# Optimization experiments

Hardware: AMD Instinct MI355X
Metric: run time of the kernel (lower is better)

Reference implementation:

```python
import jax, jax.numpy as jnp
import numpy as np

N = 50000      # nodes
E = 800000     # edges (avg degree 16)
H = 4          # attention heads
F_IN = 256     # input feature dim
D = 64         # per-head hidden/out dim (hidden*H = 256 chains into next layer)
NEG_SLOPE = 0.2  # DGL GATConv default leaky_relu slope


def setup_inputs() -> dict:
    key = jax.random.key(0)
    ks = jax.random.split(key, 12)
    inp = {
        "features": jax.random.normal(ks[0], (N, F_IN), jnp.float32),
        "src": jax.random.randint(ks[1], (E,), 0, N, jnp.int32),
        "dst": jax.random.randint(ks[2], (E,), 0, N, jnp.int32),
    }
    dims = [(F_IN, D), (H * D, D), (H * D, D)]
    for i, (fin, dout) in enumerate(dims):
        sc = 1.0 / np.sqrt(fin)
        inp[f"W{i+1}"] = jax.random.normal(ks[3 + 3 * i], (fin, H * dout), jnp.float32) * sc
        inp[f"al{i+1}"] = jax.random.normal(ks[4 + 3 * i], (H, dout), jnp.float32) * 0.1
        inp[f"ar{i+1}"] = jax.random.normal(ks[5 + 3 * i], (H, dout), jnp.float32) * 0.1
        inp[f"b{i+1}"] = jnp.zeros((H * dout,), jnp.float32)
    return inp


def gat_layer(h, src, dst, W, al, ar, b, act):
    n = h.shape[0]
    feat = (h @ W).reshape(n, H, -1)                     # [N, H, D]
    el = jnp.sum(feat * al, axis=-1)                     # [N, H]
    er = jnp.sum(feat * ar, axis=-1)                     # [N, H]
    e = jax.nn.leaky_relu(el[src] + er[dst], NEG_SLOPE)  # [E, H]
    # segment (per-dst) softmax over incoming edges
    m = jax.ops.segment_max(e, dst, num_segments=n)      # [N, H]
    ex = jnp.exp(e - m[dst])
    s = jax.ops.segment_sum(ex, dst, num_segments=n)
    alpha = ex / jnp.maximum(s[dst], 1e-9)               # [E, H]
    # weighted scatter-aggregate of source features
    out = jax.ops.segment_sum(feat[src] * alpha[..., None], dst, num_segments=n)  # [N, H, D]
    out = out + b.reshape(1, H, -1)
    if act:
        out = jax.nn.elu(out)
    return out.reshape(n, -1)                            # flatten(1): concat heads


def reference(features, src, dst, W1, al1, ar1, b1, W2, al2, ar2, b2, W3, al3, ar3, b3):
    h = gat_layer(features, src, dst, W1, al1, ar1, b1, act=True)
    h = gat_layer(h, src, dst, W2, al2, ar2, b2, act=True)
    h = gat_layer(h, src, dst, W3, al3, ar3, b3, act=False)
    return h  # [N, H*D] = [50000, 256]
```

## Files before the change

### kernel.cpp

```cpp
#include <hip/hip_runtime.h>
#include <hip/hip_bf16.h>
#include <cstdint>


#define FEAT 256
#define NHEAD 4

typedef short short8 __attribute__((ext_vector_type(8)));
typedef float f32x4 __attribute__((ext_vector_type(4)));

__device__ __forceinline__ ushort f2bf(float v) {
    uint u = __float_as_uint(v);
    uint r = (u + 0x7fffu + ((u >> 16) & 1u)) >> 16;
    return (ushort)r;
}
__device__ __forceinline__ float bf2f(ushort h) {
    return __uint_as_float(((uint)h) << 16);
}

__global__ void hist_kernel(const int* __restrict__ dst, int* __restrict__ deg, int E) {
    int e = blockIdx.x * 256 + threadIdx.x;
    if (e < E) atomicAdd(&deg[dst[e]], 1);
}

__global__ void scan_block(const int* __restrict__ deg, int* __restrict__ offs,
                           int* __restrict__ bsums, int n) {
    __shared__ int s[256];
    int i = blockIdx.x * 256 + threadIdx.x;
    int v = (i < n) ? deg[i] : 0;
    s[threadIdx.x] = v; __syncthreads();
    #pragma unroll
    for (int off = 1; off < 256; off <<= 1) {
        int t = (threadIdx.x >= off) ? s[threadIdx.x - off] : 0;
        __syncthreads();
        s[threadIdx.x] += t;
        __syncthreads();
    }
    if (i < n) offs[i] = s[threadIdx.x] - v;
    if (threadIdx.x == 255) bsums[blockIdx.x] = s[255];
}

__global__ void scan_sums(int* __restrict__ bsums, int nb) {
    __shared__ int s[256];
    int v = (threadIdx.x < nb) ? bsums[threadIdx.x] : 0;
    s[threadIdx.x] = v; __syncthreads();
    #pragma unroll
    for (int off = 1; off < 256; off <<= 1) {
        int t = (threadIdx.x >= off) ? s[threadIdx.x - off] : 0;
        __syncthreads();
        s[threadIdx.x] += t;
        __syncthreads();
    }
    if (threadIdx.x < nb) bsums[threadIdx.x] = s[threadIdx.x] - v;
}

__global__ void scan_add(int* __restrict__ offs, int* __restrict__ cursor,
                         const int* __restrict__ bsums, int n, int total) {
    int i = blockIdx.x * 256 + threadIdx.x;
    if (i < n) {
        int o = offs[i] + bsums[i >> 8];
        offs[i] = o;
        cursor[i] = o;
    }
    if (i == 0) offs[n] = total;
}

__global__ void scatter_kernel(const int* __restrict__ src, const int* __restrict__ dst,
                               int* __restrict__ cursor, int* __restrict__ csr_src, int E) {
    int e = blockIdx.x * 256 + threadIdx.x;
    if (e < E) {
        int d = dst[e];
        int pos = atomicAdd(&cursor[d], 1);
        csr_src[pos] = src[e];
    }
}

__global__ void wprep_kernel(const float* __restrict__ W,
                             ushort* __restrict__ Wh, ushort* __restrict__ Wl) {
    int n = blockIdx.x;
    int k = threadIdx.x;
    float v = W[(size_t)k * FEAT + n];
    ushort h = f2bf(v);
    float r = v - bf2f(h);
    Wh[(size_t)n * FEAT + k] = h;
    Wl[(size_t)n * FEAT + k] = f2bf(r);
}

__global__ void fsplit_kernel(const float* __restrict__ A, ushort* __restrict__ Ah,
                              ushort* __restrict__ Al, int total8) {
    int i = blockIdx.x * 256 + threadIdx.x;
    if (i >= total8) return;
    const float4* p = (const float4*)(A + (size_t)i * 8);
    float4 a = p[0], b = p[1];
    float v[8] = {a.x, a.y, a.z, a.w, b.x, b.y, b.z, b.w};
    ushort hi[8], lo[8];
    #pragma unroll
    for (int t = 0; t < 8; ++t) {
        hi[t] = f2bf(v[t]);
        lo[t] = f2bf(v[t] - bf2f(hi[t]));
    }
    *(short8*)(Ah + (size_t)i * 8) = *(short8*)hi;
    *(short8*)(Al + (size_t)i * 8) = *(short8*)lo;
}

#define GBM 64
#define GBK 32
#define LDK 40

__global__ __launch_bounds__(256) void gemm_fused(const ushort* __restrict__ Ahg,
                                                  const ushort* __restrict__ Alg,
                                                  const ushort* __restrict__ Whg,
                                                  const ushort* __restrict__ Wlg,
                                                  const float* __restrict__ alv,
                                                  const float* __restrict__ arv,
                                                  ushort* __restrict__ featB,
                                                  float* __restrict__ el,
                                                  float* __restrict__ er, int M) {
    __shared__ ushort Ah[GBM][LDK];
    __shared__ ushort Al[GBM][LDK];
    __shared__ ushort Bh[FEAT][LDK];
    __shared__ ushort Bl[FEAT][LDK];

    const int tid  = threadIdx.x;
    const int lane = tid & 63;
    const int wid  = tid >> 6;
    const int row0 = blockIdx.x * GBM;

    const int arow = tid >> 2;
    const int achk = (tid & 3) * 8;
    const int bcol = tid;

    const int fr = lane & 15;
    const int fk = (lane >> 4) * 8;
    const int q  = lane >> 4;

    f32x4 acc[4][4];
    #pragma unroll
    for (int i = 0; i < 4; ++i)
        #pragma unroll
        for (int j = 0; j < 4; ++j) {
            f32x4 z = {0.f, 0.f, 0.f, 0.f};
            acc[i][j] = z;
        }

    const short8 z8 = {0, 0, 0, 0, 0, 0, 0, 0};

    for (int k0 = 0; k0 < FEAT; k0 += GBK) {
        short8 a_h, a_l;
        if (row0 + arow < M) {
            a_h = *(const short8*)(Ahg + (size_t)(row0 + arow) * FEAT + k0 + achk);
            a_l = *(const short8*)(Alg + (size_t)(row0 + arow) * FEAT + k0 + achk);
        } else {
            a_h = z8; a_l = z8;
        }
        short8 b_h[4], b_l[4];
        #pragma unroll
        for (int c = 0; c < 4; ++c) {
            b_h[c] = *(const short8*)(Whg + (size_t)bcol * FEAT + k0 + c * 8);
            b_l[c] = *(const short8*)(Wlg + (size_t)bcol * FEAT + k0 + c * 8);
        }

        __syncthreads();
        *(short8*)&Ah[arow][achk] = a_h;
        *(short8*)&Al[arow][achk] = a_l;
        #pragma unroll
        for (int c = 0; c < 4; ++c) {
            *(short8*)&Bh[bcol][c * 8] = b_h[c];
            *(short8*)&Bl[bcol][c * 8] = b_l[c];
        }
        __syncthreads();

        short8 bfh[4], bfl[4];
        #pragma unroll
        for (int nt = 0; nt < 4; ++nt) {
            bfh[nt] = *(const short8*)&Bh[wid * 64 + nt * 16 + fr][fk];
            bfl[nt] = *(const short8*)&Bl[wid * 64 + nt * 16 + fr][fk];
        }
        #pragma unroll
        for (int mt = 0; mt < 4; ++mt) {
            short8 afh = *(const short8*)&Ah[mt * 16 + fr][fk];
            short8 afl = *(const short8*)&Al[mt * 16 + fr][fk];
            #pragma unroll
            for (int nt = 0; nt < 4; ++nt) {
                acc[mt][nt] = __builtin_amdgcn_mfma_f32_16x16x32_bf16(
                    afh, bfh[nt], acc[mt][nt], 0, 0, 0);
                acc[mt][nt] = __builtin_amdgcn_mfma_f32_16x16x32_bf16(
                    afh, bfl[nt], acc[mt][nt], 0, 0, 0);
                acc[mt][nt] = __builtin_amdgcn_mfma_f32_16x16x32_bf16(
                    afl, bfh[nt], acc[mt][nt], 0, 0, 0);
            }
        }
    }

    float al4[4], ar4[4];
    #pragma unroll
    for (int nt = 0; nt < 4; ++nt) {
        al4[nt] = alv[wid * 64 + nt * 16 + fr];
        ar4[nt] = arv[wid * 64 + nt * 16 + fr];
    }
    #pragma unroll
    for (int mt = 0; mt < 4; ++mt) {
        #pragma unroll
        for (int r = 0; r < 4; ++r) {
            int row = row0 + mt * 16 + q * 4 + r;
            bool ok = row < M;
            float pl = 0.f, pr = 0.f;
            #pragma unroll
            for (int nt = 0; nt < 4; ++nt) {
                float v = acc[mt][nt][r];
                if (ok) featB[(size_t)row * FEAT + wid * 64 + nt * 16 + fr] = f2bf(v);
                pl = fmaf(v, al4[nt], pl);
                pr = fmaf(v, ar4[nt], pr);
            }
            #pragma unroll
            for (int o = 1; o < 16; o <<= 1) {
                pl += __shfl_xor(pl, o, 64);
                pr += __shfl_xor(pr, o, 64);
            }
            if (ok && fr == 0) {
                el[(size_t)row * NHEAD + wid] = pl;
                er[(size_t)row * NHEAD + wid] = pr;
            }
        }
    }
}

__global__ __launch_bounds__(256) void agg_kernel3(const ushort* __restrict__ featB,
                                                   const float* __restrict__ el,
                                                   const float* __restrict__ er,
                                                   const int* __restrict__ offs,
                                                   const int* __restrict__ csr_src,
                                                   const float* __restrict__ bias,
                                                   float* __restrict__ outF,
                                                   ushort* __restrict__ outH,
                                                   ushort* __restrict__ outL,
                                                   int act, int n) {
    int node = blockIdx.x * 4 + (threadIdx.x >> 6);
    if (node >= n) return;
    int lane = threadIdx.x & 63;
    int h = lane >> 4;
    int j16 = lane & 15;
    int f = lane * 4;
    int start = offs[node];
    int deg = offs[node + 1] - start;
    float erh = er[node * NHEAD + h];

    float m = -1e30f, ssum = 0.f;
    float acc0 = 0.f, acc1 = 0.f, acc2 = 0.f, acc3 = 0.f;
    int sidx = (j16 < deg) ? csr_src[start + j16] : 0;

    for (int p0 = 0; p0 < deg; p0 += 16) {
        int pn = p0 + 16 + j16;
        int sidx_nx = (pn < deg) ? csr_src[start + pn] : 0;
        float e = -1e30f;
        if (p0 + j16 < deg) {
            float t = el[sidx * NHEAD + h] + erh;
            e = (t > 0.f) ? t : 0.2f * t;
        }
        float cm = e;
        #pragma unroll
        for (int o = 1; o < 16; o <<= 1) cm = fmaxf(cm, __shfl_xor(cm, o, 64));
        float newm = fmaxf(m, cm);
        float sc = __expf(m - newm);
        m = newm;
        ssum *= sc; acc0 *= sc; acc1 *= sc; acc2 *= sc; acc3 *= sc;
        float w = __expf(e - m);
        ssum += w;
        int cnt = min(16, deg - p0);
        if (cnt == 16) {
            #pragma unroll
            for (int j = 0; j < 16; ++j) {
                float wj = __shfl(w, j, 16);
                int sj = __shfl(sidx, j, 16);
                ushort4 v = *(const ushort4*)(featB + (size_t)sj * FEAT + f);
                acc0 = fmaf(wj, bf2f(v.x), acc0);
                acc1 = fmaf(wj, bf2f(v.y), acc1);
                acc2 = fmaf(wj, bf2f(v.z), acc2);
                acc3 = fmaf(wj, bf2f(v.w), acc3);
            }
        } else {
            for (int j = 0; j < cnt; ++j) {
                float wj = __shfl(w, j, 16);
                int sj = __shfl(sidx, j, 16);
                ushort4 v = *(const ushort4*)(featB + (size_t)sj * FEAT + f);
                acc0 = fmaf(wj, bf2f(v.x), acc0);
                acc1 = fmaf(wj, bf2f(v.y), acc1);
                acc2 = fmaf(wj, bf2f(v.z), acc2);
                acc3 = fmaf(wj, bf2f(v.w), acc3);
            }
        }
        sidx = sidx_nx;
    }
    float st = ssum;
    #pragma unroll
    for (int o = 1; o < 16; o <<= 1) st += __shfl_xor(st, o, 64);
    float inv = 1.f / fmaxf(st, 1e-9f);
    float4 b4 = *(const float4*)(bias + f);
    float o0 = fmaf(acc0, inv, b4.x);
    float o1 = fmaf(acc1, inv, b4.y);
    float o2 = fmaf(acc2, inv, b4.z);
    float o3 = fmaf(acc3, inv, b4.w);
    if (act) {
        o0 = (o0 > 0.f) ? o0 : expm1f(o0);
        o1 = (o1 > 0.f) ? o1 : expm1f(o1);
        o2 = (o2 > 0.f) ? o2 : expm1f(o2);
        o3 = (o3 > 0.f) ? o3 : expm1f(o3);
    }
    if (outF) {
        *((float4*)(outF + (size_t)node * FEAT + f)) = make_float4(o0, o1, o2, o3);
    } else {
        ushort4 hh, ll;
        hh.x = f2bf(o0); ll.x = f2bf(o0 - bf2f(hh.x));
        hh.y = f2bf(o1); ll.y = f2bf(o1 - bf2f(hh.y));
        hh.z = f2bf(o2); ll.z = f2bf(o2 - bf2f(hh.z));
        hh.w = f2bf(o3); ll.w = f2bf(o3 - bf2f(hh.w));
        *(ushort4*)(outH + (size_t)node * FEAT + f) = hh;
        *(ushort4*)(outL + (size_t)node * FEAT + f) = ll;
    }
}

extern "C" void kernel_launch(void* const* d_in, const int* in_sizes, int n_in,
                              void* d_out, int out_size, void* d_ws, size_t ws_size,
                              hipStream_t stream) {
    const float* features = (const float*)d_in[0];
    const int*   src      = (const int*)d_in[1];
    const int*   dst      = (const int*)d_in[2];
    const int N = in_sizes[0] / FEAT;
    const int E = in_sizes[1];

    char* ws = (char*)d_ws;
    size_t off = 0;
    auto carve = [&](size_t bytes) -> void* {
        void* p = ws + off;
        off = (off + bytes + 255) & ~(size_t)255;
        return p;
    };
    int*    deg     = (int*)carve((size_t)N * 4);
    int*    offs    = (int*)carve((size_t)(N + 1) * 4);
    int*    cursor  = (int*)carve((size_t)N * 4);
    int*    bsums   = (int*)carve(4096);
    int*    csr_src = (int*)carve((size_t)E * 4);
    float*  el      = (float*)carve((size_t)N * NHEAD * 4);
    float*  er      = (float*)carve((size_t)N * NHEAD * 4);
    ushort* featB   = (ushort*)carve((size_t)N * FEAT * 2);
    ushort* inAh    = (ushort*)carve((size_t)N * FEAT * 2);
    ushort* inAl    = (ushort*)carve((size_t)N * FEAT * 2);
    ushort* Wh[3], *Wl[3];
    for (int i = 0; i < 3; ++i) {
        Wh[i] = (ushort*)carve((size_t)FEAT * FEAT * 2);
        Wl[i] = (ushort*)carve((size_t)FEAT * FEAT * 2);
    }

    const int nbE = (E + 255) / 256;
    const int nbN = (N + 255) / 256;

    hipMemsetAsync(deg, 0, (size_t)N * 4, stream);
    hist_kernel<<<nbE, 256, 0, stream>>>(dst, deg, E);
    scan_block<<<nbN, 256, 0, stream>>>(deg, offs, bsums, N);
    scan_sums<<<1, 256, 0, stream>>>(bsums, nbN);
    scan_add<<<nbN, 256, 0, stream>>>(offs, cursor, bsums, N, E);
    scatter_kernel<<<nbE, 256, 0, stream>>>(src, dst, cursor, csr_src, E);
    wprep_kernel<<<FEAT, FEAT, 0, stream>>>((const float*)d_in[3],  Wh[0], Wl[0]);
    wprep_kernel<<<FEAT, FEAT, 0, stream>>>((const float*)d_in[7],  Wh[1], Wl[1]);
    wprep_kernel<<<FEAT, FEAT, 0, stream>>>((const float*)d_in[11], Wh[2], Wl[2]);
    const int total8 = N * FEAT / 8;
    fsplit_kernel<<<(total8 + 255) / 256, 256, 0, stream>>>(features, inAh, inAl, total8);

    const int gemmBlocks = (N + GBM - 1) / GBM;
    const int nodeBlocks = (N + 3) / 4;

    gemm_fused<<<gemmBlocks, 256, 0, stream>>>(inAh, inAl, Wh[0], Wl[0],
                                               (const float*)d_in[4], (const float*)d_in[5],
                                               featB, el, er, N);
    agg_kernel3<<<nodeBlocks, 256, 0, stream>>>(featB, el, er, offs, csr_src,
                                                (const float*)d_in[6],
                                                (float*)nullptr, inAh, inAl, 1, N);
    gemm_fused<<<gemmBlocks, 256, 0, stream>>>(inAh, inAl, Wh[1], Wl[1],
                                               (const float*)d_in[8], (const float*)d_in[9],
                                               featB, el, er, N);
    agg_kernel3<<<nodeBlocks, 256, 0, stream>>>(featB, el, er, offs, csr_src,
                                                (const float*)d_in[10],
                                                (float*)nullptr, inAh, inAl, 1, N);
    gemm_fused<<<gemmBlocks, 256, 0, stream>>>(inAh, inAl, Wh[2], Wl[2],
                                               (const float*)d_in[12], (const float*)d_in[13],
                                               featB, el, er, N);
    agg_kernel3<<<nodeBlocks, 256, 0, stream>>>(featB, el, er, offs, csr_src,
                                                (const float*)d_in[14],
                                                (float*)d_out, (ushort*)nullptr, (ushort*)nullptr, 0, N);
}
```

Measured before the change: 518.0 us.

## Use two waves per node in aggregation and load GEMM B fragments directly

The aggregation kernel now gives each node two wavefronts, each covering two heads. Each wave splits its lanes into two halves that gather alternating edges in 32-edge chunks, and the halves' partial sums are combined with a cross-half shuffle. The goal is more memory-level parallelism on the irregular feature gathers, at the cost of fewer nodes per block and extra shuffles. Separately, the GEMM drops the shared-memory staging of the weight tile and loads B fragments straight from global memory into registers, removing LDS traffic and shrinking LDS use but issuing more uncoalesced global loads per wave.

```diff
diff --git a/kernel.cpp b/kernel.cpp
--- a/kernel.cpp
+++ b/kernel.cpp
@@ -118,8 +118,6 @@
                                                   float* __restrict__ er, int M) {
     __shared__ ushort Ah[GBM][LDK];
     __shared__ ushort Al[GBM][LDK];
-    __shared__ ushort Bh[FEAT][LDK];
-    __shared__ ushort Bl[FEAT][LDK];
 
     const int tid  = threadIdx.x;
     const int lane = tid & 63;
@@ -128,7 +126,6 @@
 
     const int arow = tid >> 2;
     const int achk = (tid & 3) * 8;
-    const int bcol = tid;
 
     const int fr = lane & 15;
     const int fk = (lane >> 4) * 8;
@@ -153,29 +150,19 @@
         } else {
             a_h = z8; a_l = z8;
         }
-        short8 b_h[4], b_l[4];
-        #pragma unroll
-        for (int c = 0; c < 4; ++c) {
-            b_h[c] = *(const short8*)(Whg + (size_t)bcol * FEAT + k0 + c * 8);
-            b_l[c] = *(const short8*)(Wlg + (size_t)bcol * FEAT + k0 + c * 8);
+        short8 bfh[4], bfl[4];
+        #pragma unroll
+        for (int nt = 0; nt < 4; ++nt) {
+            size_t boff = (size_t)(wid * 64 + nt * 16 + fr) * FEAT + k0 + fk;
+            bfh[nt] = *(const short8*)(Whg + boff);
+            bfl[nt] = *(const short8*)(Wlg + boff);
         }
 
         __syncthreads();
         *(short8*)&Ah[arow][achk] = a_h;
         *(short8*)&Al[arow][achk] = a_l;
-        #pragma unroll
-        for (int c = 0; c < 4; ++c) {
-            *(short8*)&Bh[bcol][c * 8] = b_h[c];
-            *(short8*)&Bl[bcol][c * 8] = b_l[c];
-        }
-        __syncthreads();
-
-        short8 bfh[4], bfl[4];
-        #pragma unroll
-        for (int nt = 0; nt < 4; ++nt) {
-            bfh[nt] = *(const short8*)&Bh[wid * 64 + nt * 16 + fr][fk];
-            bfl[nt] = *(const short8*)&Bl[wid * 64 + nt * 16 + fr][fk];
-        }
+        __syncthreads();
+
         #pragma unroll
         for (int mt = 0; mt < 4; ++mt) {
             short8 afh = *(const short8*)&Ah[mt * 16 + fr][fk];
@@ -225,7 +212,7 @@
     }
 }
 
-__global__ __launch_bounds__(256) void agg_kernel3(const ushort* __restrict__ featB,
+__global__ __launch_bounds__(256) void agg_kernel4(const ushort* __restrict__ featB,
                                                    const float* __restrict__ el,
                                                    const float* __restrict__ er,
                                                    const int* __restrict__ offs,
@@ -235,87 +222,91 @@
                                                    ushort* __restrict__ outH,
                                                    ushort* __restrict__ outL,
                                                    int act, int n) {
-    int node = blockIdx.x * 4 + (threadIdx.x >> 6);
+    int node = blockIdx.x * 2 + (threadIdx.x >> 7);
     if (node >= n) return;
     int lane = threadIdx.x & 63;
-    int h = lane >> 4;
-    int j16 = lane & 15;
-    int f = lane * 4;
+    int wv   = (threadIdx.x >> 6) & 1;
+    int j32  = lane & 31;
+    int eh   = lane >> 5;
+    int fbase = wv * 128 + j32 * 4;
+    int acch  = j32 >> 4;
+    int srcbase = acch << 5;
+    int myh_e = wv * 2 + eh;
     int start = offs[node];
     int deg = offs[node + 1] - start;
-    float erh = er[node * NHEAD + h];
+    float erh = er[node * NHEAD + myh_e];
 
     float m = -1e30f, ssum = 0.f;
-    float acc0 = 0.f, acc1 = 0.f, acc2 = 0.f, acc3 = 0.f;
-    int sidx = (j16 < deg) ? csr_src[start + j16] : 0;
-
-    for (int p0 = 0; p0 < deg; p0 += 16) {
-        int pn = p0 + 16 + j16;
+    float a0 = 0.f, a1 = 0.f, a2 = 0.f, a3 = 0.f;
+    int sidx = (j32 < deg) ? csr_src[start + j32] : 0;
+
+    for (int p0 = 0; p0 < deg; p0 += 32) {
+        int pn = p0 + 32 + j32;
         int sidx_nx = (pn < deg) ? csr_src[start + pn] : 0;
         float e = -1e30f;
-        if (p0 + j16 < deg) {
-            float t = el[sidx * NHEAD + h] + erh;
+        if (p0 + j32 < deg) {
+            float t = el[sidx * NHEAD + myh_e] + erh;
             e = (t > 0.f) ? t : 0.2f * t;
         }
         float cm = e;
         #pragma unroll
-        for (int o = 1; o < 16; o <<= 1) cm = fmaxf(cm, __shfl_xor(cm, o, 64));
+        for (int o = 1; o < 32; o <<= 1) cm = fmaxf(cm, __shfl_xor(cm, o, 32));
         float newm = fmaxf(m, cm);
         float sc = __expf(m - newm);
         m = newm;
-        ssum *= sc; acc0 *= sc; acc1 *= sc; acc2 *= sc; acc3 *= sc;
+        float sc_acc = __shfl(sc, srcbase, 64);
+        ssum *= sc;
+        a0 *= sc_acc; a1 *= sc_acc; a2 *= sc_acc; a3 *= sc_acc;
         float w = __expf(e - m);
         ssum += w;
-        int cnt = min(16, deg - p0);
-        if (cnt == 16) {
-            #pragma unroll
-            for (int j = 0; j < 16; ++j) {
-                float wj = __shfl(w, j, 16);
-                int sj = __shfl(sidx, j, 16);
-                ushort4 v = *(const ushort4*)(featB + (size_t)sj * FEAT + f);
-                acc0 = fmaf(wj, bf2f(v.x), acc0);
-                acc1 = fmaf(wj, bf2f(v.y), acc1);
-                acc2 = fmaf(wj, bf2f(v.z), acc2);
-                acc3 = fmaf(wj, bf2f(v.w), acc3);
-            }
+        int cnt = min(32, deg - p0);
+        int iters = (cnt + 1) >> 1;
+        int wsrc = srcbase + eh;
+        for (int i = 0; i < iters; ++i) {
+            int j0 = 2 * i + eh;
+            int sj = __shfl(sidx, j0, 32);
+            float wj = __shfl(w, wsrc + 2 * i, 64);
+            ushort4 v = *(const ushort4*)(featB + (size_t)sj * FEAT + fbase);
+            a0 = fmaf(wj, bf2f(v.x), a0);
+            a1 = fmaf(wj, bf2f(v.y), a1);
+            a2 = fmaf(wj, bf2f(v.z), a2);
+            a3 = fmaf(wj, bf2f(v.w), a3);
+        }
+        sidx = sidx_nx;
+    }
+    a0 += __shfl_xor(a0, 32, 64);
+    a1 += __shfl_xor(a1, 32, 64);
+    a2 += __shfl_xor(a2, 32, 64);
+    a3 += __shfl_xor(a3, 32, 64);
+
+    float st = ssum;
+    #pragma unroll
+    for (int o = 1; o < 32; o <<= 1) st += __shfl_xor(st, o, 32);
+    st = __shfl(st, srcbase, 64);
+    if (eh == 0) {
+        float inv = 1.f / fmaxf(st, 1e-9f);
+        float4 b4 = *(const float4*)(bias + fbase);
+        float o0 = fmaf(a0, inv, b4.x);
+        float o1 = fmaf(a1, inv, b4.y);
+        float o2 = fmaf(a2, inv, b4.z);
+        float o3 = fmaf(a3, inv, b4.w);
+        if (act) {
+            o0 = (o0 > 0.f) ? o0 : expm1f(o0);
+            o1 = (o1 > 0.f) ? o1 : expm1f(o1);
+            o2 = (o2 > 0.f) ? o2 : expm1f(o2);
+            o3 = (o3 > 0.f) ? o3 : expm1f(o3);
+        }
+        if (outF) {
+            *((float4*)(outF + (size_t)node * FEAT + fbase)) = make_float4(o0, o1, o2, o3);
         } else {
-            for (int j = 0; j < cnt; ++j) {
-                float wj = __shfl(w, j, 16);
-                int sj = __shfl(sidx, j, 16);
-                ushort4 v = *(const ushort4*)(featB + (size_t)sj * FEAT + f);
-                acc0 = fmaf(wj, bf2f(v.x), acc0);
-                acc1 = fmaf(wj, bf2f(v.y), acc1);
-                acc2 = fmaf(wj, bf2f(v.z), acc2);
-                acc3 = fmaf(wj, bf2f(v.w), acc3);
-            }
-        }
-        sidx = sidx_nx;
-    }
-    float st = ssum;
-    #pragma unroll
-    for (int o = 1; o < 16; o <<= 1) st += __shfl_xor(st, o, 64);
-    float inv = 1.f / fmaxf(st, 1e-9f);
-    float4 b4 = *(const float4*)(bias + f);
-    float o0 = fmaf(acc0, inv, b4.x);
-    float o1 = fmaf(acc1, inv, b4.y);
-    float o2 = fmaf(acc2, inv, b4.z);
-    float o3 = fmaf(acc3, inv, b4.w);
-    if (act) {
-        o0 = (o0 > 0.f) ? o0 : expm1f(o0);
-        o1 = (o1 > 0.f) ? o1 : expm1f(o1);
-        o2 = (o2 > 0.f) ? o2 : expm1f(o2);
-        o3 = (o3 > 0.f) ? o3 : expm1f(o3);
-    }
-    if (outF) {
-        *((float4*)(outF + (size_t)node * FEAT + f)) = make_float4(o0, o1, o2, o3);
-    } else {
-        ushort4 hh, ll;
-        hh.x = f2bf(o0); ll.x = f2bf(o0 - bf2f(hh.x));
-        hh.y = f2bf(o1); ll.y = f2bf(o1 - bf2f(hh.y));
-        hh.z = f2bf(o2); ll.z = f2bf(o2 - bf2f(hh.z));
-        hh.w = f2bf(o3); ll.w = f2bf(o3 - bf2f(hh.w));
-        *(ushort4*)(outH + (size_t)node * FEAT + f) = hh;
-        *(ushort4*)(outL + (size_t)node * FEAT + f) = ll;
+            ushort4 hh, ll;
+            hh.x = f2bf(o0); ll.x = f2bf(o0 - bf2f(hh.x));
+            hh.y = f2bf(o1); ll.y = f2bf(o1 - bf2f(hh.y));
+            hh.z = f2bf(o2); ll.z = f2bf(o2 - bf2f(hh.z));
+            hh.w = f2bf(o3); ll.w = f2bf(o3 - bf2f(hh.w));
+            *(ushort4*)(outH + (size_t)node * FEAT + fbase) = hh;
+            *(ushort4*)(outL + (size_t)node * FEAT + fbase) = ll;
+        }
     }
 }
 
@@ -367,24 +358,24 @@
     fsplit_kernel<<<(total8 + 255) / 256, 256, 0, stream>>>(features, inAh, inAl, total8);
 
     const int gemmBlocks = (N + GBM - 1) / GBM;
-    const int nodeBlocks = (N + 3) / 4;
+    const int aggBlocks  = (N + 1) / 2;
 
     gemm_fused<<<gemmBlocks, 256, 0, stream>>>(inAh, inAl, Wh[0], Wl[0],
                                                (const float*)d_in[4], (const float*)d_in[5],
                                                featB, el, er, N);
-    agg_kernel3<<<nodeBlocks, 256, 0, stream>>>(featB, el, er, offs, csr_src,
-                                                (const float*)d_in[6],
-                                                (float*)nullptr, inAh, inAl, 1, N);
+    agg_kernel4<<<aggBlocks, 256, 0, stream>>>(featB, el, er, offs, csr_src,
+                                               (const float*)d_in[6],
+                                               (float*)nullptr, inAh, inAl, 1, N);
     gemm_fused<<<gemmBlocks, 256, 0, stream>>>(inAh, inAl, Wh[1], Wl[1],
                                                (const float*)d_in[8], (const float*)d_in[9],
                                                featB, el, er, N);
-    agg_kernel3<<<nodeBlocks, 256, 0, stream>>>(featB, el, er, offs, csr_src,
-                                                (const float*)d_in[10],
-                                                (float*)nullptr, inAh, inAl, 1, N);
+    agg_kernel4<<<aggBlocks, 256, 0, stream>>>(featB, el, er, offs, csr_src,
+                                               (const float*)d_in[10],
+                                               (float*)nullptr, inAh, inAl, 1, N);
     gemm_fused<<<gemmBlocks, 256, 0, stream>>>(inAh, inAl, Wh[2], Wl[2],
                                                (const float*)d_in[12], (const float*)d_in[13],
                                                featB, el, er, N);
-    agg_kernel3<<<nodeBlocks, 256, 0, stream>>>(featB, el, er, offs, csr_src,
-                                                (const float*)d_in[14],
-                                                (float*)d_out, (ushort*)nullptr, (ushort*)nullptr, 0, N);
-}
+    agg_kernel4<<<aggBlocks, 256, 0, stream>>>(featB, el, er, offs, csr_src,
+                                               (const float*)d_in[14],
+                                               (float*)d_out, (ushort*)nullptr, (ushort*)nullptr, 0, N);
+}
```

Result: no change. 511.2 us (-1.3%).

## Double-buffer A tiles in GEMM, read weights directly from global, merge weight prep

Applied to the files above, without the earlier changes.

The GEMM keeps only the A hi/lo tiles in LDS and double-buffers them, so the next tile's global load overlaps the MFMA work and one barrier per k-step is enough. The weight fragments are read straight from global/L2 instead of being staged through a large LDS buffer, which shrinks shared memory and should allow more resident blocks. The three weight-prep launches are folded into one grid. The tradeoff is that each block now loads B with less coalesced, repeated global reads that depend on cache hits.

```diff
diff --git a/kernel.cpp b/kernel.cpp
--- a/kernel.cpp
+++ b/kernel.cpp
@@ -75,8 +75,14 @@
     }
 }
 
-__global__ void wprep_kernel(const float* __restrict__ W,
-                             ushort* __restrict__ Wh, ushort* __restrict__ Wl) {
+__global__ void wprep3_kernel(const float* __restrict__ W0, const float* __restrict__ W1,
+                              const float* __restrict__ W2,
+                              ushort* __restrict__ Wh0, ushort* __restrict__ Wl0,
+                              ushort* __restrict__ Wh1, ushort* __restrict__ Wl1,
+                              ushort* __restrict__ Wh2, ushort* __restrict__ Wl2) {
+    const float* W = (blockIdx.y == 0) ? W0 : (blockIdx.y == 1) ? W1 : W2;
+    ushort* Wh = (blockIdx.y == 0) ? Wh0 : (blockIdx.y == 1) ? Wh1 : Wh2;
+    ushort* Wl = (blockIdx.y == 0) ? Wl0 : (blockIdx.y == 1) ? Wl1 : Wl2;
     int n = blockIdx.x;
     int k = threadIdx.x;
     float v = W[(size_t)k * FEAT + n];
@@ -106,6 +112,7 @@
 #define GBM 64
 #define GBK 32
 #define LDK 40
+#define NKIT (FEAT / GBK)
 
 __global__ __launch_bounds__(256) void gemm_fused(const ushort* __restrict__ Ahg,
                                                   const ushort* __restrict__ Alg,
@@ -116,10 +123,8 @@
                                                   ushort* __restrict__ featB,
                                                   float* __restrict__ el,
                                                   float* __restrict__ er, int M) {
-    __shared__ ushort Ah[GBM][LDK];
-    __shared__ ushort Al[GBM][LDK];
-    __shared__ ushort Bh[FEAT][LDK];
-    __shared__ ushort Bl[FEAT][LDK];
+    __shared__ ushort Ah[2][GBM][LDK];
+    __shared__ ushort Al[2][GBM][LDK];
 
     const int tid  = threadIdx.x;
     const int lane = tid & 63;
@@ -128,7 +133,9 @@
 
     const int arow = tid >> 2;
     const int achk = (tid & 3) * 8;
-    const int bcol = tid;
+    const bool aok = (row0 + arow) < M;
+    const ushort* ApH = Ahg + (size_t)(row0 + arow) * FEAT + achk;
+    const ushort* ApL = Alg + (size_t)(row0 + arow) * FEAT + achk;
 
     const int fr = lane & 15;
     const int fk = (lane >> 4) * 8;
@@ -145,41 +152,36 @@
 
     const short8 z8 = {0, 0, 0, 0, 0, 0, 0, 0};
 
-    for (int k0 = 0; k0 < FEAT; k0 += GBK) {
-        short8 a_h, a_l;
-        if (row0 + arow < M) {
-            a_h = *(const short8*)(Ahg + (size_t)(row0 + arow) * FEAT + k0 + achk);
-            a_l = *(const short8*)(Alg + (size_t)(row0 + arow) * FEAT + k0 + achk);
-        } else {
-            a_h = z8; a_l = z8;
-        }
-        short8 b_h[4], b_l[4];
-        #pragma unroll
-        for (int c = 0; c < 4; ++c) {
-            b_h[c] = *(const short8*)(Whg + (size_t)bcol * FEAT + k0 + c * 8);
-            b_l[c] = *(const short8*)(Wlg + (size_t)bcol * FEAT + k0 + c * 8);
-        }
-
-        __syncthreads();
-        *(short8*)&Ah[arow][achk] = a_h;
-        *(short8*)&Al[arow][achk] = a_l;
-        #pragma unroll
-        for (int c = 0; c < 4; ++c) {
-            *(short8*)&Bh[bcol][c * 8] = b_h[c];
-            *(short8*)&Bl[bcol][c * 8] = b_l[c];
-        }
-        __syncthreads();
-
+    {
+        short8 a_h = aok ? *(const short8*)(ApH) : z8;
+        short8 a_l = aok ? *(const short8*)(ApL) : z8;
+        *(short8*)&Ah[0][arow][achk] = a_h;
+        *(short8*)&Al[0][arow][achk] = a_l;
+    }
+
+    #pragma unroll
+    for (int t = 0; t < NKIT; ++t) {
+        const int cur = t & 1;
+        const int k0 = t * GBK;
+        short8 a_h = z8, a_l = z8;
+        if (t + 1 < NKIT && aok) {
+            a_h = *(const short8*)(ApH + k0 + GBK);
+            a_l = *(const short8*)(ApL + k0 + GBK);
+        }
         short8 bfh[4], bfl[4];
         #pragma unroll
         for (int nt = 0; nt < 4; ++nt) {
-            bfh[nt] = *(const short8*)&Bh[wid * 64 + nt * 16 + fr][fk];
-            bfl[nt] = *(const short8*)&Bl[wid * 64 + nt * 16 + fr][fk];
-        }
+            size_t boff = (size_t)(wid * 64 + nt * 16 + fr) * FEAT + k0 + fk;
+            bfh[nt] = *(const short8*)(Whg + boff);
+            bfl[nt] = *(const short8*)(Wlg + boff);
+        }
+
+        __syncthreads();
+
         #pragma unroll
         for (int mt = 0; mt < 4; ++mt) {
-            short8 afh = *(const short8*)&Ah[mt * 16 + fr][fk];
-            short8 afl = *(const short8*)&Al[mt * 16 + fr][fk];
+            short8 afh = *(const short8*)&Ah[cur][mt * 16 + fr][fk];
+            short8 afl = *(const short8*)&Al[cur][mt * 16 + fr][fk];
             #pragma unroll
             for (int nt = 0; nt < 4; ++nt) {
                 acc[mt][nt] = __builtin_amdgcn_mfma_f32_16x16x32_bf16(
@@ -189,6 +191,10 @@
                 acc[mt][nt] = __builtin_amdgcn_mfma_f32_16x16x32_bf16(
                     afl, bfh[nt], acc[mt][nt], 0, 0, 0);
             }
+        }
+        if (t + 1 < NKIT) {
+            *(short8*)&Ah[cur ^ 1][arow][achk] = a_h;
+            *(short8*)&Al[cur ^ 1][arow][achk] = a_l;
         }
     }
 
@@ -360,9 +366,10 @@
     scan_sums<<<1, 256, 0, stream>>>(bsums, nbN);
     scan_add<<<nbN, 256, 0, stream>>>(offs, cursor, bsums, N, E);
     scatter_kernel<<<nbE, 256, 0, stream>>>(src, dst, cursor, csr_src, E);
-    wprep_kernel<<<FEAT, FEAT, 0, stream>>>((const float*)d_in[3],  Wh[0], Wl[0]);
-    wprep_kernel<<<FEAT, FEAT, 0, stream>>>((const float*)d_in[7],  Wh[1], Wl[1]);
-    wprep_kernel<<<FEAT, FEAT, 0, stream>>>((const float*)d_in[11], Wh[2], Wl[2]);
+    dim3 wgrid(FEAT, 3);
+    wprep3_kernel<<<wgrid, FEAT, 0, stream>>>((const float*)d_in[3], (const float*)d_in[7],
+                                              (const float*)d_in[11],
+                                              Wh[0], Wl[0], Wh[1], Wl[1], Wh[2], Wl[2]);
     const int total8 = N * FEAT / 8;
     fsplit_kernel<<<(total8 + 255) / 256, 256, 0, stream>>>(features, inAh, inAl, total8);
 
```

Result: faster. 490.0 us (-5.4%).
